# Kernel tuning notes

Measured on AMD Instinct MI355X. Metric: run time of the kernel, lower is better.

Reference implementation:

```python
import jax, jax.numpy as jnp
import numpy as np

N = 50000
E = 800000
F_IN = 128
HID = 32
HEADS = 4
NCLS = 16
NEG_SLOPE = 0.2


def setup_inputs() -> dict:
    key = jax.random.key(0)
    ks = jax.random.split(key, 10)
    x = jax.random.normal(ks[0], (N, F_IN), dtype=jnp.float32)
    edge_index = jax.random.randint(ks[1], (2, E), 0, N, dtype=jnp.int32)
    W1 = jax.random.normal(ks[2], (F_IN, HEADS * HID), dtype=jnp.float32) * 0.1
    a_src1 = jax.random.normal(ks[3], (HEADS, HID), dtype=jnp.float32) * 0.1
    a_dst1 = jax.random.normal(ks[4], (HEADS, HID), dtype=jnp.float32) * 0.1
    b1 = jax.random.normal(ks[5], (HEADS * HID,), dtype=jnp.float32) * 0.1
    W2 = jax.random.normal(ks[6], (HEADS * HID, NCLS), dtype=jnp.float32) * 0.1
    a_src2 = jax.random.normal(ks[7], (1, NCLS), dtype=jnp.float32) * 0.1
    a_dst2 = jax.random.normal(ks[8], (1, NCLS), dtype=jnp.float32) * 0.1
    b2 = jax.random.normal(ks[9], (NCLS,), dtype=jnp.float32) * 0.1
    return {"x": x, "edge_index": edge_index, "W1": W1, "a_src1": a_src1,
            "a_dst1": a_dst1, "b1": b1, "W2": W2, "a_src2": a_src2,
            "a_dst2": a_dst2, "b2": b2}


def _gat_layer(x, src, dst, W, a_src, a_dst, bias, heads, out_dim, concat):
    n = x.shape[0]
    h = (x @ W).reshape(n, heads, out_dim)               # [N,H,D]
    al_s = jnp.einsum('nhd,hd->nh', h, a_src)            # [N,H]
    al_d = jnp.einsum('nhd,hd->nh', h, a_dst)            # [N,H]
    e = jax.nn.leaky_relu(al_s[src] + al_d[dst], NEG_SLOPE)  # [E,H]
    # segment softmax over destination nodes
    m = jax.ops.segment_max(e, dst, num_segments=n)      # [N,H]
    ex = jnp.exp(e - m[dst])                             # [E,H]
    den = jax.ops.segment_sum(ex, dst, num_segments=n)   # [N,H]
    alpha = ex / den[dst]
    msg = h[src] * alpha[:, :, None]                     # [E,H,D]
    out = jax.ops.segment_sum(msg, dst, num_segments=n)  # [N,H,D]
    if concat:
        out = out.reshape(n, heads * out_dim)
    else:
        out = out.mean(axis=1)
    return out + bias


def reference(x, edge_index, W1, a_src1, a_dst1, b1, W2, a_src2, a_dst2, b2):
    # PyG GATConv default add_self_loops=True
    loops = jnp.arange(N, dtype=edge_index.dtype)
    src = jnp.concatenate([edge_index[0], loops])
    dst = jnp.concatenate([edge_index[1], loops])
    h = _gat_layer(x, src, dst, W1, a_src1, a_dst1, b1, HEADS, HID, True)
    h = jax.nn.elu(h)
    out = _gat_layer(h, src, dst, W2, a_src2, a_dst2, b2, 1, NCLS, False)
    return jax.nn.log_softmax(out, axis=1)
```

## Files before the change

kernel.cpp:

```cpp
#include <hip/hip_runtime.h>
#include <hip/hip_bf16.h>

#define N_NODES 50000
#define N_EDGES 800000
#define ET (N_EDGES + N_NODES)
#define F_IN 128
#define HH 128
#define HEADS 4
#define HID 32
#define NCLS 16
#define NEG 0.2f
#define CAP 96
#define MAXD 64

typedef unsigned short u16;
typedef short bf16x8 __attribute__((ext_vector_type(8)));
typedef float f32x4 __attribute__((ext_vector_type(4)));
typedef u16 u16x8 __attribute__((ext_vector_type(8)));

__device__ __forceinline__ float lrelu(float x) { return x > 0.f ? x : NEG * x; }
__device__ __forceinline__ float bu2f(u16 u) { return __uint_as_float(((unsigned)u) << 16); }
__device__ __forceinline__ u16 f2bu(float f) {
    __hip_bfloat16 h = __float2bfloat16(f);
    return *reinterpret_cast<u16*>(&h);
}

__device__ __forceinline__ void edge_sd(const int* __restrict__ ei, int i, int& s, int& d) {
    if (i < N_EDGES) { s = ei[i]; d = ei[N_EDGES + i]; }
    else             { s = i - N_EDGES; d = s; }
}

__global__ void k_fill(const int* __restrict__ ei, int* __restrict__ cnt,
                       int* __restrict__ esrc) {
    int i = blockIdx.x * blockDim.x + threadIdx.x;
    if (i >= ET) return;
    int s, d; edge_sd(ei, i, s, d);
    int pos = atomicAdd(&cnt[d], 1);
    if (pos < CAP) esrc[d * CAP + pos] = s;
}

__global__ void __launch_bounds__(256) k_gemm1(
        const float* __restrict__ x, const float* __restrict__ W1,
        const float* __restrict__ a_s, const float* __restrict__ a_d,
        u16* __restrict__ h1b, float* __restrict__ al_s, float* __restrict__ al_d) {
    __shared__ u16 w1t[128 * 136];
    int t = threadIdx.x;
    for (int it = 0; it < 64; ++it) {
        int idx = it * 256 + t;
        int k = idx >> 7, n = idx & 127;
        w1t[n * 136 + k] = f2bu(W1[idx]);
    }
    __syncthreads();
    int wave = t >> 6, lane = t & 63;
    int col = lane & 15, quad = lane >> 4;
    int tb = blockIdx.x * 64 + wave * 16;
    union { bf16x8 v; u16 u[8]; } af[4];
    int anode = tb + col;
    bool aval = anode < N_NODES;
    const float* xr = x + (size_t)anode * F_IN + quad * 8;
#pragma unroll
    for (int kb = 0; kb < 4; ++kb) {
        float4 lo = aval ? ((const float4*)(xr + kb * 32))[0] : make_float4(0.f, 0.f, 0.f, 0.f);
        float4 hi = aval ? ((const float4*)(xr + kb * 32))[1] : make_float4(0.f, 0.f, 0.f, 0.f);
        af[kb].u[0] = f2bu(lo.x); af[kb].u[1] = f2bu(lo.y);
        af[kb].u[2] = f2bu(lo.z); af[kb].u[3] = f2bu(lo.w);
        af[kb].u[4] = f2bu(hi.x); af[kb].u[5] = f2bu(hi.y);
        af[kb].u[6] = f2bu(hi.z); af[kb].u[7] = f2bu(hi.w);
    }
    float ps[4][4] = {}, pd[4][4] = {};
#pragma unroll
    for (int nt = 0; nt < 8; ++nt) {
        f32x4 acc = {0.f, 0.f, 0.f, 0.f};
#pragma unroll
        for (int kb = 0; kb < 4; ++kb) {
            bf16x8 bf = *(const bf16x8*)&w1t[(nt * 16 + col) * 136 + kb * 32 + quad * 8];
            acc = __builtin_amdgcn_mfma_f32_16x16x32_bf16(af[kb].v, bf, acc, 0, 0, 0);
        }
        int feat = nt * 16 + col;
        float asv = a_s[feat], adv = a_d[feat];
        const int head = nt >> 1;
#pragma unroll
        for (int r = 0; r < 4; ++r) {
            int node = tb + quad * 4 + r;
            float v = acc[r];
            if (node < N_NODES) h1b[(size_t)node * HH + feat] = f2bu(v);
            ps[r][head] = fmaf(v, asv, ps[r][head]);
            pd[r][head] = fmaf(v, adv, pd[r][head]);
        }
    }
#pragma unroll
    for (int r = 0; r < 4; ++r)
#pragma unroll
        for (int h = 0; h < 4; ++h)
#pragma unroll
            for (int w = 1; w < 16; w <<= 1) {
                ps[r][h] += __shfl_xor(ps[r][h], w);
                pd[r][h] += __shfl_xor(pd[r][h], w);
            }
    if (col == 0) {
#pragma unroll
        for (int r = 0; r < 4; ++r) {
            int node = tb + quad * 4 + r;
            if (node < N_NODES) {
#pragma unroll
                for (int h = 0; h < 4; ++h) {
                    al_s[node * 4 + h] = ps[r][h];
                    al_d[node * 4 + h] = pd[r][h];
                }
            }
        }
    }
}

__global__ void __launch_bounds__(256) k_agg1(
        const int* __restrict__ esrc, const int* __restrict__ cnt,
        const float* __restrict__ alS, const float* __restrict__ alD,
        const u16* __restrict__ h1b, const float* __restrict__ b1,
        const float* __restrict__ W2, const float* __restrict__ a_s2,
        const float* __restrict__ a_d2,
        u16* __restrict__ h2b, float* __restrict__ alS2, float* __restrict__ alD2) {
    __shared__ float wls[4][MAXD * HEADS];
    __shared__ int   sls[4][MAXD];
    __shared__ __align__(16) float rowf[4][HH];
    __shared__ float w2t[NCLS * 132];
    __shared__ float as2s[NCLS], ad2s[NCLS];
    int t = threadIdx.x;
    for (int idx = t; idx < F_IN * NCLS; idx += 256) {
        int f = idx >> 4, c = idx & 15;
        w2t[c * 132 + f] = W2[idx];
    }
    if (t < NCLS) { as2s[t] = a_s2[t]; ad2s[t] = a_d2[t]; }
    __syncthreads();
    int wave = t >> 6, lane = t & 63;
    int n = blockIdx.x * 4 + wave;
    int off = n * CAP;
    int deg = cnt[n];
    int slot = lane & 15, h = lane >> 4;
    float ad = alD[n * 4 + h];
    float den = 0.f;
    for (int e = slot; e < deg; e += 16) {
        int s = esrc[off + e];
        float wv = __expf(lrelu(alS[s * 4 + h] + ad));
        if (e < MAXD) {
            wls[wave][e * 4 + h] = wv;
            if (h == 0) sls[wave][e] = s;
        }
        den += wv;
    }
#pragma unroll
    for (int w = 1; w < 16; w <<= 1) den += __shfl_xor(den, w);
    float inv = 1.f / den;
    int quarter = lane >> 4, fl = lane & 15;
    int hb = fl >> 2;
    float invh = __shfl(inv, hb << 4);
    float adh = alD[n * 4 + hb];
    float acc[8] = {};
    for (int e = quarter; e < deg; e += 4) {
        int s; float wv;
        if (e < MAXD) {
            s = sls[wave][e];
            wv = wls[wave][e * 4 + hb];
        } else {
            s = esrc[off + e];
            wv = __expf(lrelu(alS[s * 4 + hb] + adh));
        }
        float a = wv * invh;
        u16x8 q8 = ((const u16x8*)(h1b + (size_t)s * HH))[fl];
#pragma unroll
        for (int j = 0; j < 8; ++j)
            acc[j] = fmaf(bu2f(q8[j]), a, acc[j]);
    }
#pragma unroll
    for (int j = 0; j < 8; ++j) {
        acc[j] += __shfl_xor(acc[j], 16);
        acc[j] += __shfl_xor(acc[j], 32);
    }
    if (quarter == 0) {
        const float4* b4 = (const float4*)b1;
        float4 blo = b4[fl * 2], bhi = b4[fl * 2 + 1];
        float v[8];
        v[0] = acc[0] + blo.x; v[1] = acc[1] + blo.y;
        v[2] = acc[2] + blo.z; v[3] = acc[3] + blo.w;
        v[4] = acc[4] + bhi.x; v[5] = acc[5] + bhi.y;
        v[6] = acc[6] + bhi.z; v[7] = acc[7] + bhi.w;
#pragma unroll
        for (int j = 0; j < 8; ++j) v[j] = v[j] > 0.f ? v[j] : __expf(v[j]) - 1.f;
        ((float4*)&rowf[wave][0])[fl * 2]     = make_float4(v[0], v[1], v[2], v[3]);
        ((float4*)&rowf[wave][0])[fl * 2 + 1] = make_float4(v[4], v[5], v[6], v[7]);
    }
    int c = lane & 15, q = lane >> 4;
    float h2acc = 0.f;
#pragma unroll
    for (int i = 0; i < 32; ++i) {
        int f = i * 4 + q;
        h2acc = fmaf(rowf[wave][f], w2t[c * 132 + f], h2acc);
    }
    h2acc += __shfl_xor(h2acc, 16);
    h2acc += __shfl_xor(h2acc, 32);
    if (lane < 16) h2b[(size_t)n * NCLS + lane] = f2bu(h2acc);
    float rs = h2acc * as2s[c], rd = h2acc * ad2s[c];
#pragma unroll
    for (int w = 1; w < 16; w <<= 1) { rs += __shfl_xor(rs, w); rd += __shfl_xor(rd, w); }
    if (lane == 0) { alS2[n] = rs; alD2[n] = rd; }
}

__global__ void __launch_bounds__(256) k_agg2(
        const int* __restrict__ esrc, const int* __restrict__ cnt,
        const float* __restrict__ alS2, const float* __restrict__ alD2,
        const u16* __restrict__ h2b, const float* __restrict__ b2,
        float* __restrict__ out) {
    __shared__ float wls[4][MAXD];
    __shared__ int   sls[4][MAXD];
    int wave = threadIdx.x >> 6, lane = threadIdx.x & 63;
    int n = blockIdx.x * 4 + wave;
    int off = n * CAP;
    int deg = cnt[n];
    float ad = alD2[n];
    float den = 0.f;
    for (int e = lane; e < deg; e += 64) {
        int s = esrc[off + e];
        float wv = __expf(lrelu(alS2[s] + ad));
        if (e < MAXD) { wls[wave][e] = wv; sls[wave][e] = s; }
        den += wv;
    }
#pragma unroll
    for (int w = 1; w < 64; w <<= 1) den += __shfl_xor(den, w);
    float inv = 1.f / den;
    int sub = lane >> 3, cp = lane & 7;
    float a0 = 0.f, a1 = 0.f;
    for (int e = sub; e < deg; e += 8) {
        int s; float wv;
        if (e < MAXD) { s = sls[wave][e]; wv = wls[wave][e]; }
        else          { s = esrc[off + e]; wv = __expf(lrelu(alS2[s] + ad)); }
        float al = wv * inv;
        unsigned qq = ((const unsigned*)(h2b + (size_t)s * NCLS))[cp];
        a0 = fmaf(bu2f((u16)(qq & 0xffffu)), al, a0);
        a1 = fmaf(bu2f((u16)(qq >> 16)), al, a1);
    }
    a0 += __shfl_xor(a0, 8);  a1 += __shfl_xor(a1, 8);
    a0 += __shfl_xor(a0, 16); a1 += __shfl_xor(a1, 16);
    a0 += __shfl_xor(a0, 32); a1 += __shfl_xor(a1, 32);
    float v0 = a0 + b2[2 * cp], v1 = a1 + b2[2 * cp + 1];
    float mx = fmaxf(v0, v1);
#pragma unroll
    for (int w = 1; w < 8; w <<= 1) mx = fmaxf(mx, __shfl_xor(mx, w));
    float ex = __expf(v0 - mx) + __expf(v1 - mx);
#pragma unroll
    for (int w = 1; w < 8; w <<= 1) ex += __shfl_xor(ex, w);
    float lse = mx + __logf(ex);
    if (lane < 8) ((float2*)(out + (size_t)n * NCLS))[cp] = make_float2(v0 - lse, v1 - lse);
}

extern "C" void kernel_launch(void* const* d_in, const int* in_sizes, int n_in,
                              void* d_out, int out_size, void* d_ws, size_t ws_size,
                              hipStream_t stream) {
    const float* x   = (const float*)d_in[0];
    const int*   ei  = (const int*)d_in[1];
    const float* W1  = (const float*)d_in[2];
    const float* as1 = (const float*)d_in[3];
    const float* ad1 = (const float*)d_in[4];
    const float* b1  = (const float*)d_in[5];
    const float* W2  = (const float*)d_in[6];
    const float* as2 = (const float*)d_in[7];
    const float* ad2 = (const float*)d_in[8];
    const float* b2  = (const float*)d_in[9];
    float* out = (float*)d_out;
    char* ws = (char*)d_ws;

    u16*   h1b  = (u16*)  (ws);
    float* alS1 = (float*)(ws + 12800000);
    float* alD1 = (float*)(ws + 13600000);
    u16*   h2b  = (u16*)  (ws + 14400000);
    float* alS2 = (float*)(ws + 16000000);
    float* alD2 = (float*)(ws + 16200000);
    int*   cnt  = (int*)  (ws + 16400000);
    int*   esrc = (int*)  (ws + 16600000);

    hipMemsetAsync(cnt, 0, (size_t)N_NODES * 4, stream);
    k_fill<<<(ET + 255) / 256, 256, 0, stream>>>(ei, cnt, esrc);

    k_gemm1<<<(N_NODES + 63) / 64, 256, 0, stream>>>(x, W1, as1, ad1, h1b, alS1, alD1);
    k_agg1<<<N_NODES / 4, 256, 0, stream>>>(esrc, cnt, alS1, alD1, h1b, b1,
                                            W2, as2, ad2, h2b, alS2, alD2);
    k_agg2<<<N_NODES / 4, 256, 0, stream>>>(esrc, cnt, alS2, alD2, h2b, b2, out);
}
```

Baseline: 236.0 us.

## Fuse edge fill with GEMM1 launch, cache all CAP edges in LDS, software-pipeline gathers

Merges the edge-bucketing kernel and the first GEMM into one launch. Gemm blocks are interleaved with fill blocks (one in every five) so the atomic scatter overlaps with the MFMA work and one launch is saved. The aggregation kernels now clamp degree to CAP and keep every edge's weight and source in shared memory, which drops the fallback path that recomputed weights beyond MAXD. The gather loops are also software-pipelined to prefetch the next neighbour row before accumulating the current one. Costs are more LDS per block, and the fused kernel declares the 34 KB shared array that the fill blocks never use, which may limit occupancy.

```diff
diff --git a/kernel.cpp b/kernel.cpp
--- a/kernel.cpp
+++ b/kernel.cpp
@@ -11,7 +11,9 @@
 #define NCLS 16
 #define NEG 0.2f
 #define CAP 96
-#define MAXD 64
+
+#define GB ((N_NODES + 63) / 64)
+#define FB ((ET + 255) / 256)
 
 typedef unsigned short u16;
 typedef short bf16x8 __attribute__((ext_vector_type(8)));
@@ -30,20 +32,25 @@
     else             { s = i - N_EDGES; d = s; }
 }
 
-__global__ void k_fill(const int* __restrict__ ei, int* __restrict__ cnt,
-                       int* __restrict__ esrc) {
-    int i = blockIdx.x * blockDim.x + threadIdx.x;
-    if (i >= ET) return;
-    int s, d; edge_sd(ei, i, s, d);
-    int pos = atomicAdd(&cnt[d], 1);
-    if (pos < CAP) esrc[d * CAP + pos] = s;
-}
-
-__global__ void __launch_bounds__(256) k_gemm1(
+__global__ void __launch_bounds__(256) k_fill_gemm1(
+        const int* __restrict__ ei, int* __restrict__ cnt, int* __restrict__ esrc,
         const float* __restrict__ x, const float* __restrict__ W1,
         const float* __restrict__ a_s, const float* __restrict__ a_d,
         u16* __restrict__ h1b, float* __restrict__ al_s, float* __restrict__ al_d) {
     __shared__ u16 w1t[128 * 136];
+    int bid = blockIdx.x;
+    int q = bid / 5, r = bid - q * 5;
+    bool is_gemm = (r == 0) && (q < GB);
+    if (!is_gemm) {
+        int g = (r == 0) ? min(q, GB) : min(q + 1, GB);
+        int i = (bid - g) * 256 + threadIdx.x;
+        if (i < ET) {
+            int s, d; edge_sd(ei, i, s, d);
+            int pos = atomicAdd(&cnt[d], 1);
+            if (pos < CAP) esrc[d * CAP + pos] = s;
+        }
+        return;
+    }
     int t = threadIdx.x;
     for (int it = 0; it < 64; ++it) {
         int idx = it * 256 + t;
@@ -53,7 +60,7 @@
     __syncthreads();
     int wave = t >> 6, lane = t & 63;
     int col = lane & 15, quad = lane >> 4;
-    int tb = blockIdx.x * 64 + wave * 16;
+    int tb = q * 64 + wave * 16;
     union { bf16x8 v; u16 u[8]; } af[4];
     int anode = tb + col;
     bool aval = anode < N_NODES;
@@ -80,32 +87,32 @@
         float asv = a_s[feat], adv = a_d[feat];
         const int head = nt >> 1;
 #pragma unroll
-        for (int r = 0; r < 4; ++r) {
-            int node = tb + quad * 4 + r;
-            float v = acc[r];
+        for (int rr = 0; rr < 4; ++rr) {
+            int node = tb + quad * 4 + rr;
+            float v = acc[rr];
             if (node < N_NODES) h1b[(size_t)node * HH + feat] = f2bu(v);
-            ps[r][head] = fmaf(v, asv, ps[r][head]);
-            pd[r][head] = fmaf(v, adv, pd[r][head]);
-        }
-    }
-#pragma unroll
-    for (int r = 0; r < 4; ++r)
+            ps[rr][head] = fmaf(v, asv, ps[rr][head]);
+            pd[rr][head] = fmaf(v, adv, pd[rr][head]);
+        }
+    }
+#pragma unroll
+    for (int rr = 0; rr < 4; ++rr)
 #pragma unroll
         for (int h = 0; h < 4; ++h)
 #pragma unroll
             for (int w = 1; w < 16; w <<= 1) {
-                ps[r][h] += __shfl_xor(ps[r][h], w);
-                pd[r][h] += __shfl_xor(pd[r][h], w);
+                ps[rr][h] += __shfl_xor(ps[rr][h], w);
+                pd[rr][h] += __shfl_xor(pd[rr][h], w);
             }
     if (col == 0) {
 #pragma unroll
-        for (int r = 0; r < 4; ++r) {
-            int node = tb + quad * 4 + r;
+        for (int rr = 0; rr < 4; ++rr) {
+            int node = tb + quad * 4 + rr;
             if (node < N_NODES) {
 #pragma unroll
                 for (int h = 0; h < 4; ++h) {
-                    al_s[node * 4 + h] = ps[r][h];
-                    al_d[node * 4 + h] = pd[r][h];
+                    al_s[node * 4 + h] = ps[rr][h];
+                    al_d[node * 4 + h] = pd[rr][h];
                 }
             }
         }
@@ -119,8 +126,8 @@
         const float* __restrict__ W2, const float* __restrict__ a_s2,
         const float* __restrict__ a_d2,
         u16* __restrict__ h2b, float* __restrict__ alS2, float* __restrict__ alD2) {
-    __shared__ float wls[4][MAXD * HEADS];
-    __shared__ int   sls[4][MAXD];
+    __shared__ float wls[4][CAP * HEADS];
+    __shared__ int   sls[4][CAP];
     __shared__ __align__(16) float rowf[4][HH];
     __shared__ float w2t[NCLS * 132];
     __shared__ float as2s[NCLS], ad2s[NCLS];
@@ -134,17 +141,15 @@
     int wave = t >> 6, lane = t & 63;
     int n = blockIdx.x * 4 + wave;
     int off = n * CAP;
-    int deg = cnt[n];
+    int deg = min(cnt[n], CAP);
     int slot = lane & 15, h = lane >> 4;
     float ad = alD[n * 4 + h];
     float den = 0.f;
     for (int e = slot; e < deg; e += 16) {
         int s = esrc[off + e];
         float wv = __expf(lrelu(alS[s * 4 + h] + ad));
-        if (e < MAXD) {
-            wls[wave][e * 4 + h] = wv;
-            if (h == 0) sls[wave][e] = s;
-        }
+        wls[wave][e * 4 + h] = wv;
+        if (h == 0) sls[wave][e] = s;
         den += wv;
     }
 #pragma unroll
@@ -153,19 +158,21 @@
     int quarter = lane >> 4, fl = lane & 15;
     int hb = fl >> 2;
     float invh = __shfl(inv, hb << 4);
-    float adh = alD[n * 4 + hb];
     float acc[8] = {};
-    for (int e = quarter; e < deg; e += 4) {
-        int s; float wv;
-        if (e < MAXD) {
-            s = sls[wave][e];
-            wv = wls[wave][e * 4 + hb];
-        } else {
-            s = esrc[off + e];
-            wv = __expf(lrelu(alS[s * 4 + hb] + adh));
-        }
-        float a = wv * invh;
+    int e = quarter;
+    if (e < deg) {
+        int s = sls[wave][e];
+        float a = wls[wave][e * 4 + hb] * invh;
         u16x8 q8 = ((const u16x8*)(h1b + (size_t)s * HH))[fl];
+        for (e += 4; e < deg; e += 4) {
+            int s2 = sls[wave][e];
+            float a2 = wls[wave][e * 4 + hb] * invh;
+            u16x8 q8n = ((const u16x8*)(h1b + (size_t)s2 * HH))[fl];
+#pragma unroll
+            for (int j = 0; j < 8; ++j)
+                acc[j] = fmaf(bu2f(q8[j]), a, acc[j]);
+            q8 = q8n; a = a2;
+        }
 #pragma unroll
         for (int j = 0; j < 8; ++j)
             acc[j] = fmaf(bu2f(q8[j]), a, acc[j]);
@@ -188,11 +195,11 @@
         ((float4*)&rowf[wave][0])[fl * 2]     = make_float4(v[0], v[1], v[2], v[3]);
         ((float4*)&rowf[wave][0])[fl * 2 + 1] = make_float4(v[4], v[5], v[6], v[7]);
     }
-    int c = lane & 15, q = lane >> 4;
+    int c = lane & 15, qq2 = lane >> 4;
     float h2acc = 0.f;
 #pragma unroll
     for (int i = 0; i < 32; ++i) {
-        int f = i * 4 + q;
+        int f = i * 4 + qq2;
         h2acc = fmaf(rowf[wave][f], w2t[c * 132 + f], h2acc);
     }
     h2acc += __shfl_xor(h2acc, 16);
@@ -209,18 +216,18 @@
         const float* __restrict__ alS2, const float* __restrict__ alD2,
         const u16* __restrict__ h2b, const float* __restrict__ b2,
         float* __restrict__ out) {
-    __shared__ float wls[4][MAXD];
-    __shared__ int   sls[4][MAXD];
+    __shared__ float wls[4][CAP];
+    __shared__ int   sls[4][CAP];
     int wave = threadIdx.x >> 6, lane = threadIdx.x & 63;
     int n = blockIdx.x * 4 + wave;
     int off = n * CAP;
-    int deg = cnt[n];
+    int deg = min(cnt[n], CAP);
     float ad = alD2[n];
     float den = 0.f;
     for (int e = lane; e < deg; e += 64) {
         int s = esrc[off + e];
         float wv = __expf(lrelu(alS2[s] + ad));
-        if (e < MAXD) { wls[wave][e] = wv; sls[wave][e] = s; }
+        wls[wave][e] = wv; sls[wave][e] = s;
         den += wv;
     }
 #pragma unroll
@@ -228,14 +235,21 @@
     float inv = 1.f / den;
     int sub = lane >> 3, cp = lane & 7;
     float a0 = 0.f, a1 = 0.f;
-    for (int e = sub; e < deg; e += 8) {
-        int s; float wv;
-        if (e < MAXD) { s = sls[wave][e]; wv = wls[wave][e]; }
-        else          { s = esrc[off + e]; wv = __expf(lrelu(alS2[s] + ad)); }
-        float al = wv * inv;
-        unsigned qq = ((const unsigned*)(h2b + (size_t)s * NCLS))[cp];
-        a0 = fmaf(bu2f((u16)(qq & 0xffffu)), al, a0);
-        a1 = fmaf(bu2f((u16)(qq >> 16)), al, a1);
+    int e = sub;
+    if (e < deg) {
+        int s = sls[wave][e];
+        float al = wls[wave][e] * inv;
+        unsigned qv = ((const unsigned*)(h2b + (size_t)s * NCLS))[cp];
+        for (e += 8; e < deg; e += 8) {
+            int s2 = sls[wave][e];
+            float al2 = wls[wave][e] * inv;
+            unsigned qn = ((const unsigned*)(h2b + (size_t)s2 * NCLS))[cp];
+            a0 = fmaf(bu2f((u16)(qv & 0xffffu)), al, a0);
+            a1 = fmaf(bu2f((u16)(qv >> 16)), al, a1);
+            qv = qn; al = al2;
+        }
+        a0 = fmaf(bu2f((u16)(qv & 0xffffu)), al, a0);
+        a1 = fmaf(bu2f((u16)(qv >> 16)), al, a1);
     }
     a0 += __shfl_xor(a0, 8);  a1 += __shfl_xor(a1, 8);
     a0 += __shfl_xor(a0, 16); a1 += __shfl_xor(a1, 16);
@@ -277,9 +291,8 @@
     int*   esrc = (int*)  (ws + 16600000);
 
     hipMemsetAsync(cnt, 0, (size_t)N_NODES * 4, stream);
-    k_fill<<<(ET + 255) / 256, 256, 0, stream>>>(ei, cnt, esrc);
-
-    k_gemm1<<<(N_NODES + 63) / 64, 256, 0, stream>>>(x, W1, as1, ad1, h1b, alS1, alD1);
+    k_fill_gemm1<<<GB + FB, 256, 0, stream>>>(ei, cnt, esrc,
+                                              x, W1, as1, ad1, h1b, alS1, alD1);
     k_agg1<<<N_NODES / 4, 256, 0, stream>>>(esrc, cnt, alS1, alD1, h1b, b1,
                                             W2, as2, ad2, h2b, alS2, alD2);
     k_agg2<<<N_NODES / 4, 256, 0, stream>>>(esrc, cnt, alS2, alD2, h2b, b2, out);
```

Result: faster. 215.9 us (median of 2 runs) (-8.5%).
